# Performance work log

Hardware: AMD Instinct MI355X
Metric: run time of the kernel (lower is better)

The kernel has to match this reference:

```python
import jax, jax.numpy as jnp
import numpy as np


def setup_inputs() -> dict:
    key = jax.random.key(0)
    k1, k2 = jax.random.split(key)
    B, S, D_IN, D_OUT = 4, 2048, 2048, 8192
    x = jax.random.normal(k1, (B, S, D_IN), dtype=jnp.float32)
    # kaiming_normal_ fan_out, linear: std = 1/sqrt(fan_out)
    weight = jax.random.normal(k2, (D_OUT, D_IN), dtype=jnp.float32) * (1.0 / np.sqrt(D_OUT))
    return {"x": x, "weight": weight}


def reference(x, weight):
    # Per-output-row mean-abs scale, clamped
    scale = jnp.clip(jnp.mean(jnp.abs(weight), axis=1, keepdims=True), 1e-5, None)  # [out, 1]
    w_q = jnp.clip(jnp.round(weight / scale), -1.0, 1.0)  # ternary {-1, 0, 1}
    # STE: value = w_q * scale, gradient flows to weight as identity
    w = weight + jax.lax.stop_gradient(w_q * scale - weight)  # [out, in]
    # F.linear: x @ w.T
    return jnp.einsum('bsi,oi->bso', x, w)
```

## Files before the change

kernel.cpp:

```cpp
#include <hip/hip_runtime.h>
#include <hip/hip_bf16.h>
#include <stdint.h>


typedef float  floatx4 __attribute__((ext_vector_type(4)));
typedef _Float16 f16x8 __attribute__((ext_vector_type(8)));
typedef _Float16 f16x4 __attribute__((ext_vector_type(4)));

#define BM 128
#define BN 128
#define BK 32

__global__ __launch_bounds__(256) void quant_weight(
    const float* __restrict__ W, f16x4* __restrict__ Q,
    float* __restrict__ scale, int K )
{
    const int wave = threadIdx.x >> 6;
    const int lane = threadIdx.x & 63;
    const int row  = blockIdx.x * 4 + wave;

    const float4* row4 = (const float4*)(W + (size_t)row * K);
    float4 v[8];
    float s = 0.f;
    #pragma unroll
    for (int i = 0; i < 8; ++i) {
        v[i] = row4[lane + 64 * i];
        s += fabsf(v[i].x) + fabsf(v[i].y) + fabsf(v[i].z) + fabsf(v[i].w);
    }
    #pragma unroll
    for (int m = 1; m < 64; m <<= 1) s += __shfl_xor(s, m, 64);

    const float sc  = fmaxf(s / (float)K, 1e-5f);
    if (lane == 0) scale[row] = sc;
    const float inv = 1.0f / sc;

    f16x4* qrow = Q + (size_t)row * (K / 4);
    #pragma unroll
    for (int i = 0; i < 8; ++i) {
        float t[4] = {v[i].x, v[i].y, v[i].z, v[i].w};
        f16x4 o;
        #pragma unroll
        for (int j = 0; j < 4; ++j)
            o[j] = (_Float16)fminf(fmaxf(rintf(t[j] * inv), -1.f), 1.f);
        qrow[lane + 64 * i] = o;
    }
}

__global__ __launch_bounds__(256) void cvt_f16(
    const float4* __restrict__ X, f16x4* __restrict__ Y)
{
    const size_t i = (size_t)blockIdx.x * blockDim.x + threadIdx.x;
    float4 a = X[i];
    f16x4 o;
    o[0] = (_Float16)a.x; o[1] = (_Float16)a.y;
    o[2] = (_Float16)a.z; o[3] = (_Float16)a.w;
    Y[i] = o;
}

__device__ inline void gload_lds16(const void* g, void* l) {
    __builtin_amdgcn_global_load_lds(
        (const __attribute__((address_space(1))) void*)g,
        (__attribute__((address_space(3))) void*)l, 16, 0, 0);
}

__global__ __launch_bounds__(256) void gemm_bt_scaled(
    const _Float16* __restrict__ A,
    const _Float16* __restrict__ B,
    const float* __restrict__ scale,
    float* __restrict__ C,
    int M, int N, int K)
{
    __shared__ __align__(16) _Float16 sA[BM * BK];
    __shared__ __align__(16) _Float16 sB[BN * BK];

    const int tid  = threadIdx.x;
    const int lane = tid & 63;
    const int wv   = tid >> 6;
    const int wm   = wv & 1;
    const int wn   = wv >> 1;
    const int rowA0 = blockIdx.y * BM;
    const int rowB0 = blockIdx.x * BN;

    const int lrow  = lane & 15;
    const int kquad = lane >> 4;

    floatx4 acc[4][4] = {};

    int aoff[4], boff[4];
    #pragma unroll
    for (int t = 0; t < 4; ++t) {
        int ra = wm * 64 + t * 16 + lrow;
        int rb = wn * 64 + t * 16 + lrow;
        aoff[t] = (ra * 4 + (kquad ^ ((ra >> 1) & 3))) * 8;
        boff[t] = (rb * 4 + (kquad ^ ((rb >> 1) & 3))) * 8;
    }

    for (int kk = 0; kk < K; kk += BK) {
        #pragma unroll
        for (int j = 0; j < 2; ++j) {
            int c = tid + 256 * j;
            int row = c >> 2;
            int kc  = (c & 3) ^ ((row >> 1) & 3);
            gload_lds16(A + (size_t)(rowA0 + row) * K + kk + kc * 8, &sA[c * 8]);
        }
        #pragma unroll
        for (int j = 0; j < 2; ++j) {
            int c = tid + 256 * j;
            int row = c >> 2;
            int kc  = (c & 3) ^ ((row >> 1) & 3);
            gload_lds16(B + (size_t)(rowB0 + row) * K + kk + kc * 8, &sB[c * 8]);
        }
        __syncthreads();

        f16x8 af[4], bfr[4];
        #pragma unroll
        for (int mt = 0; mt < 4; ++mt) af[mt]  = *(const f16x8*)&sA[aoff[mt]];
        #pragma unroll
        for (int nt = 0; nt < 4; ++nt) bfr[nt] = *(const f16x8*)&sB[boff[nt]];

        #pragma unroll
        for (int mt = 0; mt < 4; ++mt)
            #pragma unroll
            for (int nt = 0; nt < 4; ++nt)
                acc[mt][nt] = __builtin_amdgcn_mfma_f32_16x16x32_f16(
                    af[mt], bfr[nt], acc[mt][nt], 0, 0, 0);
        __syncthreads();
    }

    const int colb = rowB0 + wn * 64 + lrow;
    const int rowb = rowA0 + wm * 64 + kquad * 4;
    #pragma unroll
    for (int nt = 0; nt < 4; ++nt) {
        const float sc = scale[colb + nt * 16];
        #pragma unroll
        for (int mt = 0; mt < 4; ++mt) {
            #pragma unroll
            for (int r = 0; r < 4; ++r) {
                C[(size_t)(rowb + mt * 16 + r) * N + colb + nt * 16] =
                    acc[mt][nt][r] * sc;
            }
        }
    }
}

extern "C" void kernel_launch(void* const* d_in, const int* in_sizes, int n_in,
                              void* d_out, int out_size, void* d_ws, size_t ws_size,
                              hipStream_t stream) {
    const float* x = (const float*)d_in[0];
    const float* w = (const float*)d_in[1];
    float* out = (float*)d_out;

    const int M = 8192, K = 2048, N = 8192;

    char* ws = (char*)d_ws;
    float*     scale = (float*)ws;
    _Float16*  Xh    = (_Float16*)(ws + 32768);
    _Float16*  Qh    = (_Float16*)(ws + 32768 + (size_t)M * K * 2);

    quant_weight<<<N / 4, 256, 0, stream>>>(w, (f16x4*)Qh, scale, K);
    cvt_f16<<<(M * K / 4) / 256, 256, 0, stream>>>((const float4*)x, (f16x4*)Xh);
    gemm_bt_scaled<<<dim3(N / BN, M / BM), 256, 0, stream>>>(Xh, Qh, scale, out, M, N, K);
}
```

Before: 654.1 us.

## Use 256x256 tiles with 4-slot LDS pipeline, 512 threads, XCD-aware block swizzle

```diff
diff --git a/kernel.cpp b/kernel.cpp
--- a/kernel.cpp
+++ b/kernel.cpp
@@ -7,9 +7,10 @@
 typedef _Float16 f16x8 __attribute__((ext_vector_type(8)));
 typedef _Float16 f16x4 __attribute__((ext_vector_type(4)));
 
-#define BM 128
-#define BN 128
+#define BM 256
+#define BN 256
 #define BK 32
+#define NSLOT 4
 
 __global__ __launch_bounds__(256) void quant_weight(
     const float* __restrict__ W, f16x4* __restrict__ Q,
@@ -63,77 +64,135 @@
         (__attribute__((address_space(3))) void*)l, 16, 0, 0);
 }
 
-__global__ __launch_bounds__(256) void gemm_bt_scaled(
+__global__ __launch_bounds__(512, 2) void gemm_bt_scaled(
     const _Float16* __restrict__ A,
     const _Float16* __restrict__ B,
     const float* __restrict__ scale,
     float* __restrict__ C,
     int M, int N, int K)
 {
-    __shared__ __align__(16) _Float16 sA[BM * BK];
-    __shared__ __align__(16) _Float16 sB[BN * BK];
+    __shared__ __align__(16) _Float16 lds[NSLOT][2][BM * BK];
 
     const int tid  = threadIdx.x;
     const int lane = tid & 63;
     const int wv   = tid >> 6;
-    const int wm   = wv & 1;
-    const int wn   = wv >> 1;
-    const int rowA0 = blockIdx.y * BM;
-    const int rowB0 = blockIdx.x * BN;
+    const int wm   = wv >> 2;
+    const int wn   = wv & 3;
+
+    const int nwg = gridDim.x;
+    const int cpx = nwg >> 3;
+    const int id  = blockIdx.x;
+    const int swz = (id & 7) * cpx + (id >> 3);
+    const int nbx = N / BN;
+    const int by  = swz / nbx;
+    const int bx  = swz % nbx;
+    const int rowA0 = by * BM;
+    const int rowB0 = bx * BN;
 
     const int lrow  = lane & 15;
     const int kquad = lane >> 4;
 
-    floatx4 acc[4][4] = {};
-
-    int aoff[4], boff[4];
+    floatx4 acc[8][4] = {};
+
+    int aoff[8], boff[4];
+    #pragma unroll
+    for (int t = 0; t < 8; ++t) {
+        int ra = wm * 128 + t * 16 + lrow;
+        aoff[t] = (ra * 4 + (kquad ^ ((ra >> 1) & 3))) * 8;
+    }
     #pragma unroll
     for (int t = 0; t < 4; ++t) {
-        int ra = wm * 64 + t * 16 + lrow;
         int rb = wn * 64 + t * 16 + lrow;
-        aoff[t] = (ra * 4 + (kquad ^ ((ra >> 1) & 3))) * 8;
         boff[t] = (rb * 4 + (kquad ^ ((rb >> 1) & 3))) * 8;
     }
 
-    for (int kk = 0; kk < K; kk += BK) {
+    const int c0 = tid,        c1 = tid + 512;
+    const int r0 = c0 >> 2,    r1 = c1 >> 2;
+    const int k0 = (c0 & 3) ^ ((r0 >> 1) & 3);
+    const int k1 = (c1 & 3) ^ ((r1 >> 1) & 3);
+    const _Float16* pa0 = A + (size_t)(rowA0 + r0) * K + k0 * 8;
+    const _Float16* pa1 = A + (size_t)(rowA0 + r1) * K + k1 * 8;
+    const _Float16* pb0 = B + (size_t)(rowB0 + r0) * K + k0 * 8;
+    const _Float16* pb1 = B + (size_t)(rowB0 + r1) * K + k1 * 8;
+    const int eo0 = c0 * 8, eo1 = c1 * 8;
+
+    #pragma unroll
+    for (int t = 0; t < 3; ++t) {
+        gload_lds16(pa0 + t * BK, &lds[t][0][eo0]);
+        gload_lds16(pa1 + t * BK, &lds[t][0][eo1]);
+        gload_lds16(pb0 + t * BK, &lds[t][1][eo0]);
+        gload_lds16(pb1 + t * BK, &lds[t][1][eo1]);
+    }
+    pa0 += 3 * BK; pa1 += 3 * BK; pb0 += 3 * BK; pb1 += 3 * BK;
+
+    asm volatile("s_waitcnt vmcnt(8)" ::: "memory");
+    __builtin_amdgcn_s_barrier();
+
+    const int NT = K / BK;
+    for (int kt0 = 0; kt0 < NT; kt0 += NSLOT) {
         #pragma unroll
-        for (int j = 0; j < 2; ++j) {
-            int c = tid + 256 * j;
-            int row = c >> 2;
-            int kc  = (c & 3) ^ ((row >> 1) & 3);
-            gload_lds16(A + (size_t)(rowA0 + row) * K + kk + kc * 8, &sA[c * 8]);
+        for (int s = 0; s < NSLOT; ++s) {
+            const int kt = kt0 + s;
+            const bool st = (kt + 3 < NT);
+            const int d = (s + 3) & 3;
+
+            f16x8 afr[4], bfr[4];
+            #pragma unroll
+            for (int t = 0; t < 4; ++t) bfr[t] = *(const f16x8*)&lds[s][1][boff[t]];
+            #pragma unroll
+            for (int t = 0; t < 4; ++t) afr[t] = *(const f16x8*)&lds[s][0][aoff[t]];
+            if (st) {
+                gload_lds16(pa0, &lds[d][0][eo0]);
+                gload_lds16(pa1, &lds[d][0][eo1]);
+            }
+            __builtin_amdgcn_s_barrier();
+            asm volatile("s_waitcnt lgkmcnt(0)" ::: "memory");
+            __builtin_amdgcn_s_setprio(1);
+            #pragma unroll
+            for (int mt = 0; mt < 4; ++mt)
+                #pragma unroll
+                for (int nt = 0; nt < 4; ++nt)
+                    acc[mt][nt] = __builtin_amdgcn_mfma_f32_16x16x32_f16(
+                        afr[mt], bfr[nt], acc[mt][nt], 0, 0, 0);
+            __builtin_amdgcn_s_setprio(0);
+            __builtin_amdgcn_s_barrier();
+
+            #pragma unroll
+            for (int t = 0; t < 4; ++t) afr[t] = *(const f16x8*)&lds[s][0][aoff[t + 4]];
+            if (st) {
+                gload_lds16(pb0, &lds[d][1][eo0]);
+                gload_lds16(pb1, &lds[d][1][eo1]);
+                pa0 += BK; pa1 += BK; pb0 += BK; pb1 += BK;
+            }
+            __builtin_amdgcn_s_barrier();
+            asm volatile("s_waitcnt lgkmcnt(0)" ::: "memory");
+            __builtin_amdgcn_s_setprio(1);
+            #pragma unroll
+            for (int mt = 0; mt < 4; ++mt)
+                #pragma unroll
+                for (int nt = 0; nt < 4; ++nt)
+                    acc[mt + 4][nt] = __builtin_amdgcn_mfma_f32_16x16x32_f16(
+                        afr[mt], bfr[nt], acc[mt + 4][nt], 0, 0, 0);
+            __builtin_amdgcn_s_setprio(0);
+
+            if (kt + 3 < NT) {
+                asm volatile("s_waitcnt vmcnt(8)" ::: "memory");
+            } else if (kt + 2 < NT) {
+                asm volatile("s_waitcnt vmcnt(4)" ::: "memory");
+            } else {
+                asm volatile("s_waitcnt vmcnt(0)" ::: "memory");
+            }
+            __builtin_amdgcn_s_barrier();
         }
-        #pragma unroll
-        for (int j = 0; j < 2; ++j) {
-            int c = tid + 256 * j;
-            int row = c >> 2;
-            int kc  = (c & 3) ^ ((row >> 1) & 3);
-            gload_lds16(B + (size_t)(rowB0 + row) * K + kk + kc * 8, &sB[c * 8]);
-        }
-        __syncthreads();
-
-        f16x8 af[4], bfr[4];
-        #pragma unroll
-        for (int mt = 0; mt < 4; ++mt) af[mt]  = *(const f16x8*)&sA[aoff[mt]];
-        #pragma unroll
-        for (int nt = 0; nt < 4; ++nt) bfr[nt] = *(const f16x8*)&sB[boff[nt]];
-
-        #pragma unroll
-        for (int mt = 0; mt < 4; ++mt)
-            #pragma unroll
-            for (int nt = 0; nt < 4; ++nt)
-                acc[mt][nt] = __builtin_amdgcn_mfma_f32_16x16x32_f16(
-                    af[mt], bfr[nt], acc[mt][nt], 0, 0, 0);
-        __syncthreads();
     }
 
     const int colb = rowB0 + wn * 64 + lrow;
-    const int rowb = rowA0 + wm * 64 + kquad * 4;
+    const int rowb = rowA0 + wm * 128 + kquad * 4;
     #pragma unroll
     for (int nt = 0; nt < 4; ++nt) {
         const float sc = scale[colb + nt * 16];
         #pragma unroll
-        for (int mt = 0; mt < 4; ++mt) {
+        for (int mt = 0; mt < 8; ++mt) {
             #pragma unroll
             for (int r = 0; r < 4; ++r) {
                 C[(size_t)(rowb + mt * 16 + r) * N + colb + nt * 16] =
@@ -159,5 +218,6 @@
 
     quant_weight<<<N / 4, 256, 0, stream>>>(w, (f16x4*)Qh, scale, K);
     cvt_f16<<<(M * K / 4) / 256, 256, 0, stream>>>((const float4*)x, (f16x4*)Xh);
-    gemm_bt_scaled<<<dim3(N / BN, M / BM), 256, 0, stream>>>(Xh, Qh, scale, out, M, N, K);
-}
+    gemm_bt_scaled<<<dim3((M / BM) * (N / BN)), 512, 0, stream>>>(
+        Xh, Qh, scale, out, M, N, K);
+}
```

Result: faster. 616.5 us (-5.7%).
